# Performance work log

Hardware: AMD Instinct MI355X
Metric: run time of the kernel (lower is better)

The kernel has to match this reference:

```python
import jax, jax.numpy as jnp
import numpy as np

B, C, IMG, P = 8, 6, 384, 16
DIM, HEADS, DEPTH, MLP, NCLS = 768, 12, 4, 3072, 1000
N = (IMG // P) ** 2            # 576 patches
DH = DIM // HEADS              # 64
PATCH_DIM = C * P * P          # 1536


def setup_inputs() -> dict:
    key = jax.random.key(0)
    ks = jax.random.split(key, 13)
    f = lambda k, shp, s=0.02: jax.random.normal(k, shp, jnp.float32) * s
    return {
        "x": jax.random.normal(ks[0], (B, C, IMG, IMG), jnp.float32),
        "patch_w": f(ks[1], (PATCH_DIM, DIM)),
        "patch_b": f(ks[2], (DIM,)),
        "ln1_g": jnp.ones((DEPTH, DIM), jnp.float32),
        "ln1_b": jnp.zeros((DEPTH, DIM), jnp.float32),
        "w_qkv": f(ks[3], (DEPTH, DIM, 3 * DIM)),
        "bias_att": f(ks[4], (DEPTH, HEADS, N, N), 0.5),
        "w_out": f(ks[5], (DEPTH, DIM, DIM)),
        "ln2_g": jnp.ones((DEPTH, DIM), jnp.float32),
        "ln2_b": jnp.zeros((DEPTH, DIM), jnp.float32),
        "w1": f(ks[6], (DEPTH, DIM, MLP)),
        "b1": f(ks[7], (DEPTH, MLP)),
        "w2": f(ks[8], (DEPTH, MLP, DIM)),
        "b2": f(ks[9], (DEPTH, DIM)),
        "lnh_g": jnp.ones((DIM,), jnp.float32),
        "lnh_b": jnp.zeros((DIM,), jnp.float32),
        "w_head": f(ks[10], (DIM, NCLS)),
        "b_head": f(ks[11], (NCLS,)),
    }


def _ln(x, g, b, eps=1e-5):
    m = x.mean(-1, keepdims=True)
    v = ((x - m) ** 2).mean(-1, keepdims=True)
    return (x - m) * jax.lax.rsqrt(v + eps) * g + b


def _patchify(x, patch_w, patch_b):
    # Rearrange 'b c (h p1) (w p2) -> b (h w) (p1 p2 c)' then Linear(patch_dim, dim)
    b = x.shape[0]
    g = IMG // P
    x = x.reshape(b, C, g, P, g, P).transpose(0, 2, 4, 3, 5, 1).reshape(b, g * g, PATCH_DIM)
    return x @ patch_w + patch_b


def _forward(x, patch_w, patch_b, ln1_g, ln1_b, w_qkv, bias_att, w_out,
             ln2_g, ln2_b, w1, b1, w2, b2, lnh_g, lnh_b, w_head, b_head):
    scale = DH ** -0.5
    tok = _patchify(x, patch_w, patch_b)  # [B, N, DIM]; pos_info='mul_att_normed' -> no pos_embed added

    def block(t, p):
        l1g, l1b, wqkv, bias, wout, l2g, l2b, ww1, bb1, ww2, bb2 = p
        h = _ln(t, l1g, l1b)
        qkv = h @ wqkv                                     # [B, N, 3*DIM]
        q, k, v = jnp.split(qkv, 3, axis=-1)
        rs = lambda a: a.reshape(t.shape[0], N, HEADS, DH).transpose(0, 2, 1, 3)
        q, k, v = rs(q), rs(k), rs(v)                      # [B, H, N, DH]
        dots = jnp.einsum('bhid,bhjd->bhij', q, k) * scale
        # mul_att_normed: softmax(qk) * softmax(bias), renormalized over keys
        attn = jax.nn.softmax(dots, axis=-1) * jax.nn.softmax(bias, axis=-1)[None]
        attn = attn / attn.sum(-1, keepdims=True)
        o = jnp.einsum('bhij,bhjd->bhid', attn, v)
        o = o.transpose(0, 2, 1, 3).reshape(t.shape[0], N, DIM) @ wout
        t = t + o
        h2 = _ln(t, l2g, l2b)
        t = t + (jax.nn.gelu(h2 @ ww1 + bb1, approximate=False) @ ww2 + bb2)
        return t, None

    tok, _ = jax.lax.scan(block, tok,
                          (ln1_g, ln1_b, w_qkv, bias_att, w_out,
                           ln2_g, ln2_b, w1, b1, w2, b2))
    pooled = tok.mean(axis=1)                              # mean-pool tokens
    return _ln(pooled, lnh_g, lnh_b) @ w_head + b_head     # [B, NCLS]


def reference(x, patch_w, patch_b, ln1_g, ln1_b, w_qkv, bias_att, w_out,
              ln2_g, ln2_b, w1, b1, w2, b2, lnh_g, lnh_b, w_head, b_head):
    return _forward(x, patch_w, patch_b, ln1_g, ln1_b, w_qkv, bias_att, w_out,
                    ln2_g, ln2_b, w1, b1, w2, b2, lnh_g, lnh_b, w_head, b_head)
```

## Files before the change

### kernel.cpp

```cpp
#include <hip/hip_runtime.h>
#include <hip/hip_bf16.h>

typedef __attribute__((ext_vector_type(8))) short bf16x8;
typedef __attribute__((ext_vector_type(4))) float f32x4;

#define DEVI __device__ __forceinline__

DEVI unsigned short f2bf_bits(float f) {
    __hip_bfloat16 h = __float2bfloat16(f);
    return *reinterpret_cast<unsigned short*>(&h);
}
DEVI float bfbits2f(unsigned short u) {
    __hip_bfloat16 h = *reinterpret_cast<__hip_bfloat16*>(&u);
    return __bfloat162float(h);
}

DEVI void gload_lds16(const void* g, void* lds) {
    __builtin_amdgcn_global_load_lds(
        (const __attribute__((address_space(1))) unsigned int*)g,
        (__attribute__((address_space(3))) unsigned int*)lds, 16, 0, 0);
}

template <int N> DEVI void wait_vm() {
    if constexpr (N == 0) asm volatile("s_waitcnt vmcnt(0)" ::: "memory");
    else if constexpr (N == 6) asm volatile("s_waitcnt vmcnt(6)" ::: "memory");
    else if constexpr (N == 12) asm volatile("s_waitcnt vmcnt(12)" ::: "memory");
    __builtin_amdgcn_sched_barrier(0);
}

DEVI int2 remap2d(int bid, int total, int gx) {
    int q = total >> 3, r = total & 7, x = bid & 7, l = bid >> 3;
    int seq = (x < r ? x * (q + 1) : r * (q + 1) + (x - r) * q) + l;
    int g4 = seq / (4 * gx);
    int rem = seq - g4 * 4 * gx;
    return {g4 * 4 + (rem & 3), rem >> 2};
}

__global__ __launch_bounds__(256) void patchify_kernel(const float* __restrict__ x,
                                                       unsigned short* __restrict__ patches)
{
    size_t t8 = (size_t)blockIdx.x * 256 + threadIdx.x;
    int jq = (int)(t8 % 48);
    size_t t = t8 / 48;
    int r = (int)(t % 384); t /= 384;
    int c = (int)(t % 6);
    int b = (int)(t / 6);
    int j = jq * 8;
    int gh = r >> 4, p1 = r & 15, gw = j >> 4, p2 = j & 15;
    int prow = b * 576 + gh * 24 + gw;
    int pcol = c * 256 + p1 * 16 + p2;
    const float* src = x + ((((size_t)b * 6 + c) * 384 + r) * 384 + j);
    float4 v0 = ((const float4*)src)[0];
    float4 v1 = ((const float4*)src)[1];
    ushort u[8] = { f2bf_bits(v0.x), f2bf_bits(v0.y), f2bf_bits(v0.z), f2bf_bits(v0.w),
                    f2bf_bits(v1.x), f2bf_bits(v1.y), f2bf_bits(v1.z), f2bf_bits(v1.w) };
    *(int4*)&patches[(size_t)prow * 1536 + pcol] = *(int4*)u;
}

__global__ __launch_bounds__(256) void convT_patch_kernel(const float* __restrict__ W,
                                                          __hip_bfloat16* __restrict__ Wt)
{
    __shared__ float tile[32][33];
    int n0 = blockIdx.x * 32, kp0 = blockIdx.y * 32;
    int tx = threadIdx.x & 31, ty = threadIdx.x >> 5;
#pragma unroll
    for (int i = 0; i < 4; i++) {
        int kp = kp0 + ty + 8 * i;
        int k = (kp & 255) * 6 + (kp >> 8);
        tile[ty + 8 * i][tx] = W[(size_t)k * 768 + n0 + tx];
    }
    __syncthreads();
#pragma unroll
    for (int i = 0; i < 4; i++)
        Wt[(size_t)(n0 + ty + 8 * i) * 1536 + kp0 + tx] = __float2bfloat16(tile[tx][ty + 8 * i]);
}

DEVI void convT_body(const float* __restrict__ W, __hip_bfloat16* __restrict__ Wt,
                     int K, int N, int k0, int n0, int tid)
{
    __shared__ float tile[32][33];
    int tx = tid & 31, ty = tid >> 5;
#pragma unroll
    for (int i = 0; i < 4; i++)
        tile[ty + 8 * i][tx] = W[(size_t)(k0 + ty + 8 * i) * N + n0 + tx];
    __syncthreads();
#pragma unroll
    for (int i = 0; i < 4; i++)
        Wt[(size_t)(n0 + ty + 8 * i) * K + k0 + tx] = __float2bfloat16(tile[tx][ty + 8 * i]);
}

__global__ __launch_bounds__(256) void convT4_kernel(const float* __restrict__ wqkv,
                                                     const float* __restrict__ wout,
                                                     const float* __restrict__ w1,
                                                     const float* __restrict__ w2,
                                                     __hip_bfloat16* __restrict__ dst)
{
    int bt = blockIdx.x;
    const float* W; __hip_bfloat16* Wt; int K, N, lt;
    if (bt < 1728)      { W = wqkv; K = 768;  N = 2304; lt = bt;        Wt = dst; }
    else if (bt < 2304) { W = wout; K = 768;  N = 768;  lt = bt - 1728; Wt = dst + 1769472; }
    else if (bt < 4608) { W = w1;   K = 768;  N = 3072; lt = bt - 2304; Wt = dst + 2359296; }
    else                { W = w2;   K = 3072; N = 768;  lt = bt - 4608; Wt = dst + 4718592; }
    int tn = N >> 5;
    convT_body(W, Wt, K, N, (lt / tn) * 32, (lt % tn) * 32, threadIdx.x);
}

DEVI float ld_ln(const float* p) { return *p; }
DEVI float ld_ln(const __hip_bfloat16* p) { return __bfloat162float(*p); }
DEVI void st_ln(float* p, float v) { *p = v; }
DEVI void st_ln(__hip_bfloat16* p, float v) { *p = __float2bfloat16(v); }

template <typename InT, typename OutT>
__global__ __launch_bounds__(256) void ln_kernel(const InT* __restrict__ x,
                                                 const float* __restrict__ g,
                                                 const float* __restrict__ b,
                                                 OutT* __restrict__ out)
{
    int row = blockIdx.x, tid = threadIdx.x;
    const InT* xr = x + (size_t)row * 768;
    float v0 = ld_ln(&xr[tid]), v1 = ld_ln(&xr[tid + 256]), v2 = ld_ln(&xr[tid + 512]);
    float s = v0 + v1 + v2;
    float s2 = v0 * v0 + v1 * v1 + v2 * v2;
#pragma unroll
    for (int m = 32; m >= 1; m >>= 1) { s += __shfl_xor(s, m); s2 += __shfl_xor(s2, m); }
    __shared__ float red[8];
    int w = tid >> 6;
    if ((tid & 63) == 0) { red[w] = s; red[4 + w] = s2; }
    __syncthreads();
    s = red[0] + red[1] + red[2] + red[3];
    s2 = red[4] + red[5] + red[6] + red[7];
    float mean = s * (1.0f / 768.0f);
    float var = s2 * (1.0f / 768.0f) - mean * mean;
    float rstd = rsqrtf(var + 1e-5f);
    OutT* orow = out + (size_t)row * 768;
    st_ln(&orow[tid], (v0 - mean) * rstd * g[tid] + b[tid]);
    st_ln(&orow[tid + 256], (v1 - mean) * rstd * g[tid + 256] + b[tid + 256]);
    st_ln(&orow[tid + 512], (v2 - mean) * rstd * g[tid + 512] + b[tid + 512]);
}

template <bool BIAS, bool RESID>
__global__ __launch_bounds__(256, 2) void gemm_bt_kernel(
    const __hip_bfloat16* __restrict__ A,
    const __hip_bfloat16* __restrict__ Bt,
    const float* __restrict__ bias,
    const __hip_bfloat16* __restrict__ resid,
    __hip_bfloat16* __restrict__ Cb,
    int M, int N, int K, int gx)
{
    constexpr int BM = 64, SL = 6;
    __shared__ __align__(16) __hip_bfloat16 As[3][BM * 64];
    __shared__ __align__(16) __hip_bfloat16 Bs[3][128 * 64];
    const int tid = threadIdx.x;
    const int wid = tid >> 6, lane = tid & 63;
    const int g = lane >> 4, l16 = lane & 15;
    const int wm = (wid >> 1) * 32, wn = (wid & 1) * 64;

    int2 bc = remap2d(blockIdx.x, gridDim.x, gx);
    const int bm = bc.x * BM, bn = bc.y * 128;

    const int sr32 = tid >> 3, ci = tid & 7;
    const int cg = ci ^ (sr32 & 7);
    const int sdst = tid * 8;
    size_t aOff[2], bOff[4];
#pragma unroll
    for (int i = 0; i < 2; i++) aOff[i] = (size_t)(bm + i * 32 + sr32) * K + cg * 8;
#pragma unroll
    for (int i = 0; i < 4; i++) bOff[i] = (size_t)(bn + i * 32 + sr32) * K + cg * 8;

    auto stage = [&](__hip_bfloat16* asb, __hip_bfloat16* bsb, int tq) {
        const __hip_bfloat16* ap = A + tq * 64;
        const __hip_bfloat16* bp = Bt + tq * 64;
#pragma unroll
        for (int i = 0; i < 2; i++) gload_lds16(ap + aOff[i], asb + i * 2048 + sdst);
#pragma unroll
        for (int i = 0; i < 4; i++) gload_lds16(bp + bOff[i], bsb + i * 2048 + sdst);
    };

    f32x4 acc[2][4] = {};
    const int nt = K >> 6;

    stage(As[0], Bs[0], 0);
    stage(As[1], Bs[1], 1);
    stage(As[2], Bs[2], 2);
    wait_vm<2 * SL>();
    __builtin_amdgcn_s_barrier();
    __builtin_amdgcn_sched_barrier(0);

    for (int t = 0; t < nt; t += 3) {
#pragma unroll
        for (int u = 0; u < 3; u++) {
            const int tc = t + u;
            bf16x8 af[2][2], bfr[2][4];
#pragma unroll
            for (int s = 0; s < 2; s++) {
                const int cp = ((s * 4 + g) ^ (l16 & 7)) << 3;
#pragma unroll
                for (int mi = 0; mi < 2; mi++)
                    af[s][mi] = *(const bf16x8*)&As[u][(wm + mi * 16 + l16) * 64 + cp];
#pragma unroll
                for (int ni = 0; ni < 4; ni++)
                    bfr[s][ni] = *(const bf16x8*)&Bs[u][(wn + ni * 16 + l16) * 64 + cp];
            }
#pragma unroll
            for (int s = 0; s < 2; s++)
#pragma unroll
                for (int mi = 0; mi < 2; mi++)
#pragma unroll
                    for (int ni = 0; ni < 4; ni++)
                        acc[mi][ni] = __builtin_amdgcn_mfma_f32_16x16x32_bf16(af[s][mi], bfr[s][ni], acc[mi][ni], 0, 0, 0);

            asm volatile("s_waitcnt lgkmcnt(0)" ::: "memory");
            __builtin_amdgcn_sched_barrier(0);
            __builtin_amdgcn_s_barrier();
            __builtin_amdgcn_sched_barrier(0);

            if (tc + 3 < nt) stage(As[u], Bs[u], tc + 3);
            if (tc + 1 < nt) {
                if (tc + 4 <= nt)      wait_vm<2 * SL>();
                else if (tc + 3 == nt) wait_vm<SL>();
                else                   wait_vm<0>();
                __builtin_amdgcn_s_barrier();
                __builtin_amdgcn_sched_barrier(0);
            }
        }
    }

    __hip_bfloat16* scr = &As[0][0] + wid * (16 * 72);
#pragma unroll
    for (int mi = 0; mi < 2; mi++) {
#pragma unroll
        for (int ni = 0; ni < 4; ni++) {
            float bval = 0.0f;
            if (BIAS) bval = bias[bn + wn + ni * 16 + l16];
#pragma unroll
            for (int r = 0; r < 4; r++)
                scr[(4 * g + r) * 72 + ni * 16 + l16] = __float2bfloat16(acc[mi][ni][r] + bval);
        }
        asm volatile("s_waitcnt lgkmcnt(0)" ::: "memory");
        __builtin_amdgcn_sched_barrier(0);
#pragma unroll
        for (int q2 = 0; q2 < 2; q2++) {
            int row16 = q2 * 8 + (lane >> 3), ch = lane & 7;
            bf16x8 vv = *(const bf16x8*)&scr[row16 * 72 + ch * 8];
            int grow = bm + wm + mi * 16 + row16;
            size_t off = (size_t)grow * N + bn + wn + ch * 8;
            if (RESID) {
                bf16x8 rv = *(const bf16x8*)&resid[off];
#pragma unroll
                for (int e = 0; e < 8; e++)
                    vv[e] = (short)f2bf_bits(bfbits2f((unsigned short)vv[e]) + bfbits2f((unsigned short)rv[e]));
            }
            *(int4*)&Cb[off] = *(int4*)&vv;
        }
        asm volatile("s_waitcnt lgkmcnt(0)" ::: "memory");
        __builtin_amdgcn_sched_barrier(0);
    }
}

template <bool BIAS, bool GELU>
__global__ __launch_bounds__(256, 2) void gemm_wide_kernel(
    const __hip_bfloat16* __restrict__ A,
    const __hip_bfloat16* __restrict__ Bt,
    const float* __restrict__ bias,
    __hip_bfloat16* __restrict__ Cb,
    int M, int N, int K, int gx)
{
    constexpr int SL = 6;
    __shared__ __align__(16) __hip_bfloat16 As[3][128 * 32];
    __shared__ __align__(16) __hip_bfloat16 Bs[3][256 * 32];
    const int tid = threadIdx.x;
    const int wid = tid >> 6, lane = tid & 63;
    const int g = lane >> 4, l16 = lane & 15;
    const int wm = (wid >> 1) * 64, wn = (wid & 1) * 128;

    int2 bc = remap2d(blockIdx.x, gridDim.x, gx);
    const int bm = bc.x * 128, bn = bc.y * 256;

    const int sr = tid >> 2;
    const int csrc = (lane & 3) ^ ((lane >> 3) & 3);
    const int sdst = sr * 32 + (lane & 3) * 8;
    size_t aOff[2], bOff[4];
#pragma unroll
    for (int i = 0; i < 2; i++) aOff[i] = (size_t)(bm + i * 64 + sr) * K + csrc * 8;
#pragma unroll
    for (int i = 0; i < 4; i++) bOff[i] = (size_t)(bn + i * 64 + sr) * K + csrc * 8;

    auto stage = [&](__hip_bfloat16* asb, __hip_bfloat16* bsb, int tq) {
        const __hip_bfloat16* ap = A + tq * 32;
        const __hip_bfloat16* bp = Bt + tq * 32;
#pragma unroll
        for (int i = 0; i < 2; i++) gload_lds16(ap + aOff[i], asb + i * 2048 + sdst);
#pragma unroll
        for (int i = 0; i < 4; i++) gload_lds16(bp + bOff[i], bsb + i * 2048 + sdst);
    };

    const int pSw = (l16 >> 1) & 3;
    f32x4 acc[4][8] = {};
    const int nt = K >> 5;

    stage(As[0], Bs[0], 0);
    stage(As[1], Bs[1], 1);
    stage(As[2], Bs[2], 2);
    wait_vm<2 * SL>();
    __builtin_amdgcn_s_barrier();
    __builtin_amdgcn_sched_barrier(0);

    for (int t = 0; t < nt; t += 3) {
#pragma unroll
        for (int u = 0; u < 3; u++) {
            const int tc = t + u;
            bf16x8 af[4], bfr[8];
#pragma unroll
            for (int mi = 0; mi < 4; mi++)
                af[mi] = *(const bf16x8*)&As[u][(wm + mi * 16 + l16) * 32 + ((g ^ pSw) << 3)];
#pragma unroll
            for (int ni = 0; ni < 8; ni++)
                bfr[ni] = *(const bf16x8*)&Bs[u][(wn + ni * 16 + l16) * 32 + ((g ^ pSw) << 3)];
#pragma unroll
            for (int mi = 0; mi < 4; mi++)
#pragma unroll
                for (int ni = 0; ni < 8; ni++)
                    acc[mi][ni] = __builtin_amdgcn_mfma_f32_16x16x32_bf16(af[mi], bfr[ni], acc[mi][ni], 0, 0, 0);

            asm volatile("s_waitcnt lgkmcnt(0)" ::: "memory");
            __builtin_amdgcn_sched_barrier(0);
            __builtin_amdgcn_s_barrier();
            __builtin_amdgcn_sched_barrier(0);

            if (tc + 3 < nt) stage(As[u], Bs[u], tc + 3);
            if (tc + 1 < nt) {
                if (tc + 4 <= nt)      wait_vm<2 * SL>();
                else if (tc + 3 == nt) wait_vm<SL>();
                else                   wait_vm<0>();
                __builtin_amdgcn_s_barrier();
                __builtin_amdgcn_sched_barrier(0);
            }
        }
    }

    __hip_bfloat16* scr = &As[0][0] + wid * (16 * 136);
#pragma unroll
    for (int mi = 0; mi < 4; mi++) {
#pragma unroll
        for (int ni = 0; ni < 8; ni++) {
            float bval = 0.0f;
            if (BIAS) bval = bias[bn + wn + ni * 16 + l16];
#pragma unroll
            for (int r = 0; r < 4; r++) {
                float v = acc[mi][ni][r] + bval;
                if (GELU) v = 0.5f * v * (1.0f + erff(v * 0.70710678118654752f));
                scr[(4 * g + r) * 136 + ni * 16 + l16] = __float2bfloat16(v);
            }
        }
        asm volatile("s_waitcnt lgkmcnt(0)" ::: "memory");
        __builtin_amdgcn_sched_barrier(0);
#pragma unroll
        for (int q2 = 0; q2 < 4; q2++) {
            int idx = q2 * 64 + lane;
            int row16 = idx >> 4, ch = idx & 15;
            bf16x8 vv = *(const bf16x8*)&scr[row16 * 136 + ch * 8];
            int grow = bm + wm + mi * 16 + row16;
            *(int4*)&Cb[(size_t)grow * N + bn + wn + ch * 8] = *(int4*)&vv;
        }
        asm volatile("s_waitcnt lgkmcnt(0)" ::: "memory");
        __builtin_amdgcn_sched_barrier(0);
    }
}

__global__ __launch_bounds__(256) void attn_kernel(const __hip_bfloat16* __restrict__ qkvb,
                                                   const float* __restrict__ bias,
                                                   unsigned short* __restrict__ o)
{
    const int seq = (blockIdx.x & 7) * 108 + (blockIdx.x >> 3);
    const int bb = seq & 7, qt = (seq >> 3) % 9, h = seq / 72;
    const int q0 = qt * 64;
    const int tid = threadIdx.x;
    const int wq = tid >> 6, lane = tid & 63, g = lane >> 4, l16 = lane & 15;

    __shared__ __align__(16) unsigned short Qs[64 * 72];
    __shared__ __align__(16) unsigned short Ks[64 * 72];
    __shared__ __align__(16) unsigned short Vt[64 * 72];
    __shared__ __align__(16) unsigned short Ps[4][16 * 72];

    {
        int r = tid >> 2, cb = (tid & 3) * 16;
        const int4* s4 = (const int4*)&qkvb[(size_t)(bb * 576 + q0 + r) * 2304 + h * 64 + cb];
        int4* d4 = (int4*)&Qs[r * 72 + cb];
        d4[0] = s4[0]; d4[1] = s4[1];
    }
    __syncthreads();
    bf16x8 qf0 = *(const bf16x8*)&Qs[(wq * 16 + l16) * 72 + g * 8];
    bf16x8 qf1 = *(const bf16x8*)&Qs[(wq * 16 + l16) * 72 + 32 + g * 8];

    float m_r[4] = {-1e30f, -1e30f, -1e30f, -1e30f};
    float l_r[4] = {0.f, 0.f, 0.f, 0.f};
    f32x4 oa[4] = {};
    const float* bias_h = bias + (size_t)h * 576 * 576;
    const float scale = 0.125f;

    for (int kt = 0; kt < 576; kt += 64) {
        {
            int r = tid >> 2, cb = (tid & 3) * 16;
            const int4* s4 = (const int4*)&qkvb[(size_t)(bb * 576 + kt + r) * 2304 + 768 + h * 64 + cb];
            int4* d4 = (int4*)&Ks[r * 72 + cb];
            d4[0] = s4[0]; d4[1] = s4[1];
            int key = tid & 63, d0 = (tid >> 6) * 16;
            const unsigned short* vs = (const unsigned short*)&qkvb[(size_t)(bb * 576 + kt + key) * 2304 + 1536 + h * 64 + d0];
            bf16x8 v0 = *(const bf16x8*)vs;
            bf16x8 v1 = *(const bf16x8*)(vs + 8);
#pragma unroll
            for (int e = 0; e < 8; e++) {
                Vt[(d0 + e) * 72 + key] = (unsigned short)v0[e];
                Vt[(d0 + 8 + e) * 72 + key] = (unsigned short)v1[e];
            }
        }
        __syncthreads();

        float bl[4][4];
#pragma unroll
        for (int kc = 0; kc < 4; kc++)
#pragma unroll
            for (int r = 0; r < 4; r++) {
                int q = q0 + wq * 16 + 4 * g + r;
                bl[kc][r] = bias_h[(size_t)q * 576 + kt + kc * 16 + l16];
            }

        f32x4 sc[4] = {};
        __builtin_amdgcn_s_setprio(1);
#pragma unroll
        for (int kc = 0; kc < 4; kc++) {
            bf16x8 kf0 = *(const bf16x8*)&Ks[(kc * 16 + l16) * 72 + g * 8];
            bf16x8 kf1 = *(const bf16x8*)&Ks[(kc * 16 + l16) * 72 + 32 + g * 8];
            sc[kc] = __builtin_amdgcn_mfma_f32_16x16x32_bf16(qf0, kf0, sc[kc], 0, 0, 0);
            sc[kc] = __builtin_amdgcn_mfma_f32_16x16x32_bf16(qf1, kf1, sc[kc], 0, 0, 0);
        }
        __builtin_amdgcn_s_setprio(0);

        float sv[4][4], mt[4] = {-1e30f, -1e30f, -1e30f, -1e30f};
#pragma unroll
        for (int kc = 0; kc < 4; kc++)
#pragma unroll
            for (int r = 0; r < 4; r++) {
                float s = sc[kc][r] * scale + bl[kc][r];
                sv[kc][r] = s;
                mt[r] = fmaxf(mt[r], s);
            }
#pragma unroll
        for (int r = 0; r < 4; r++)
#pragma unroll
            for (int m = 1; m < 16; m <<= 1) mt[r] = fmaxf(mt[r], __shfl_xor(mt[r], m));

        float sf[4];
#pragma unroll
        for (int r = 0; r < 4; r++) {
            float mn = fmaxf(m_r[r], mt[r]);
            sf[r] = __expf(m_r[r] - mn);
            m_r[r] = mn;
        }
        float rs[4] = {0.f, 0.f, 0.f, 0.f};
#pragma unroll
        for (int kc = 0; kc < 4; kc++)
#pragma unroll
            for (int r = 0; r < 4; r++) {
                float p = __expf(sv[kc][r] - m_r[r]);
                rs[r] += p;
                Ps[wq][(4 * g + r) * 72 + kc * 16 + l16] = f2bf_bits(p);
            }
#pragma unroll
        for (int r = 0; r < 4; r++) {
#pragma unroll
            for (int m = 1; m < 16; m <<= 1) rs[r] += __shfl_xor(rs[r], m);
            l_r[r] = l_r[r] * sf[r] + rs[r];
        }
#pragma unroll
        for (int dt = 0; dt < 4; dt++)
#pragma unroll
            for (int r = 0; r < 4; r++) oa[dt][r] *= sf[r];

        asm volatile("s_waitcnt lgkmcnt(0)" ::: "memory");

        __builtin_amdgcn_s_setprio(1);
#pragma unroll
        for (int s = 0; s < 2; s++) {
            bf16x8 pf = *(const bf16x8*)&Ps[wq][l16 * 72 + s * 32 + g * 8];
#pragma unroll
            for (int dt = 0; dt < 4; dt++) {
                bf16x8 vf = *(const bf16x8*)&Vt[(dt * 16 + l16) * 72 + s * 32 + g * 8];
                oa[dt] = __builtin_amdgcn_mfma_f32_16x16x32_bf16(pf, vf, oa[dt], 0, 0, 0);
            }
        }
        __builtin_amdgcn_s_setprio(0);
        __syncthreads();
    }

#pragma unroll
    for (int dt = 0; dt < 4; dt++)
#pragma unroll
        for (int r = 0; r < 4; r++) {
            int q = q0 + wq * 16 + 4 * g + r;
            float v = oa[dt][r] / l_r[r];
            o[(size_t)(bb * 576 + q) * 768 + h * 64 + dt * 16 + l16] = f2bf_bits(v);
        }
}

__global__ __launch_bounds__(256) void pool_kernel(const __hip_bfloat16* __restrict__ tok,
                                                   float* __restrict__ pooled)
{
    int d = blockIdx.x * 256 + threadIdx.x;
    int b = blockIdx.y;
    float s = 0.0f;
    for (int n = 0; n < 576; n++) s += __bfloat162float(tok[(size_t)(b * 576 + n) * 768 + d]);
    pooled[b * 768 + d] = s * (1.0f / 576.0f);
}

__global__ __launch_bounds__(256) void head_kernel(const float* __restrict__ lnp,
                                                   const float* __restrict__ w,
                                                   const float* __restrict__ bh,
                                                   float* __restrict__ out)
{
    int c = blockIdx.x * 256 + threadIdx.x;
    int b = blockIdx.y;
    if (c >= 1000) return;
    float s = bh[c];
    for (int d = 0; d < 768; d++) s += lnp[b * 768 + d] * w[(size_t)d * 1000 + c];
    out[b * 1000 + c] = s;
}

extern "C" void kernel_launch(void* const* d_in, const int* in_sizes, int n_in,
                              void* d_out, int out_size, void* d_ws, size_t ws_size,
                              hipStream_t stream)
{
    const float* x = (const float*)d_in[0];
    const float* patch_w = (const float*)d_in[1];
    const float* patch_b = (const float*)d_in[2];
    const float* ln1_g = (const float*)d_in[3];
    const float* ln1_b = (const float*)d_in[4];
    const float* w_qkv = (const float*)d_in[5];
    const float* bias_att = (const float*)d_in[6];
    const float* w_out = (const float*)d_in[7];
    const float* ln2_g = (const float*)d_in[8];
    const float* ln2_b = (const float*)d_in[9];
    const float* w1 = (const float*)d_in[10];
    const float* b1 = (const float*)d_in[11];
    const float* w2 = (const float*)d_in[12];
    const float* b2 = (const float*)d_in[13];
    const float* lnh_g = (const float*)d_in[14];
    const float* lnh_b = (const float*)d_in[15];
    const float* w_head = (const float*)d_in[16];
    const float* b_head = (const float*)d_in[17];
    float* out = (float*)d_out;

    char* ws = (char*)d_ws;
    __hip_bfloat16* tok = (__hip_bfloat16*)(ws + 0);
    __hip_bfloat16* qkv_bf = (__hip_bfloat16*)(ws + 14155776);
    float* pooled = (float*)(ws + 56623104);
    float* pooledln = (float*)(ws + 56647680);
    __hip_bfloat16* patches = (__hip_bfloat16*)(ws + 56672256);
    __hip_bfloat16* lw = patches;
    __hip_bfloat16* h_bf = (__hip_bfloat16*)(ws + 70828032);
    __hip_bfloat16* o_bf = (__hip_bfloat16*)(ws + 77905920);
    __hip_bfloat16* hid_bf = (__hip_bfloat16*)(ws + 84983808);
    __hip_bfloat16* wbuf = (__hip_bfloat16*)(ws + 113295360);

    patchify_kernel<<<3456, 256, 0, stream>>>(x, (unsigned short*)patches);
    convT_patch_kernel<<<dim3(24, 48), 256, 0, stream>>>(patch_w, wbuf);
    gemm_bt_kernel<true, false><<<432, 256, 0, stream>>>(
        patches, wbuf, patch_b, nullptr, tok, 4608, 768, 1536, 6);

    for (int l = 0; l < 4; l++) {
        convT4_kernel<<<6912, 256, 0, stream>>>(
            w_qkv + (size_t)l * 768 * 2304, w_out + (size_t)l * 768 * 768,
            w1 + (size_t)l * 768 * 3072, w2 + (size_t)l * 3072 * 768, lw);
        ln_kernel<__hip_bfloat16, __hip_bfloat16><<<4608, 256, 0, stream>>>(
            tok, ln1_g + l * 768, ln1_b + l * 768, h_bf);
        gemm_wide_kernel<false, false><<<324, 256, 0, stream>>>(
            h_bf, lw, nullptr, qkv_bf, 4608, 2304, 768, 9);
        attn_kernel<<<864, 256, 0, stream>>>(
            qkv_bf, bias_att + (size_t)l * 12 * 576 * 576, (unsigned short*)o_bf);
        gemm_bt_kernel<false, true><<<432, 256, 0, stream>>>(
            o_bf, lw + 1769472, nullptr, tok, tok, 4608, 768, 768, 6);
        ln_kernel<__hip_bfloat16, __hip_bfloat16><<<4608, 256, 0, stream>>>(
            tok, ln2_g + l * 768, ln2_b + l * 768, h_bf);
        gemm_wide_kernel<true, true><<<432, 256, 0, stream>>>(
            h_bf, lw + 2359296, b1 + l * 3072, hid_bf, 4608, 3072, 768, 12);
        gemm_bt_kernel<true, true><<<432, 256, 0, stream>>>(
            hid_bf, lw + 4718592, b2 + l * 768, tok, tok, 4608, 768, 3072, 6);
    }

    pool_kernel<<<dim3(3, 8), 256, 0, stream>>>(tok, pooled);
    ln_kernel<float, float><<<8, 256, 0, stream>>>(pooled, lnh_g, lnh_b, pooledln);
    head_kernel<<<dim3(4, 8), 256, 0, stream>>>(pooledln, w_head, b_head, out);
}
```

Baseline: 845.4 us.

## Replace wide GEMM with 256x256 eight-wave ping-pong pipelined GEMM kernel

Adds gemm_8ph_kernel, a 512-thread, 256x256-tile GEMM that splits each K=64 step into two 32-wide halves in double-buffered LDS. It interleaves global-to-LDS staging of the next halves with four MFMA phases, separated by barriers and s_setprio. It replaces gemm_wide_kernel for the QKV and MLP-up GEMMs, halving the block count. The goal is more reuse per tile and overlap of loads with compute. The cost is fewer blocks (162/216 on 256 CUs, under one wave) and a heavier register footprint.

```diff
diff --git a/kernel.cpp b/kernel.cpp
--- a/kernel.cpp
+++ b/kernel.cpp
@@ -23,8 +23,13 @@
 
 template <int N> DEVI void wait_vm() {
     if constexpr (N == 0) asm volatile("s_waitcnt vmcnt(0)" ::: "memory");
+    else if constexpr (N == 4) asm volatile("s_waitcnt vmcnt(4)" ::: "memory");
     else if constexpr (N == 6) asm volatile("s_waitcnt vmcnt(6)" ::: "memory");
     else if constexpr (N == 12) asm volatile("s_waitcnt vmcnt(12)" ::: "memory");
+    __builtin_amdgcn_sched_barrier(0);
+}
+DEVI void lgkm0() {
+    asm volatile("s_waitcnt lgkmcnt(0)" ::: "memory");
     __builtin_amdgcn_sched_barrier(0);
 }
 
@@ -34,6 +39,13 @@
     int g4 = seq / (4 * gx);
     int rem = seq - g4 * 4 * gx;
     return {g4 * 4 + (rem & 3), rem >> 2};
+}
+DEVI int2 remap2d_g2(int bid, int total, int gx) {
+    int q = total >> 3, r = total & 7, x = bid & 7, l = bid >> 3;
+    int seq = (x < r ? x * (q + 1) : r * (q + 1) + (x - r) * q) + l;
+    int g2 = seq / (2 * gx);
+    int rem = seq - g2 * 2 * gx;
+    return {g2 * 2 + (rem & 1), rem >> 1};
 }
 
 __global__ __launch_bounds__(256) void patchify_kernel(const float* __restrict__ x,
@@ -138,6 +150,152 @@
     st_ln(&orow[tid + 512], (v2 - mean) * rstd * g[tid + 512] + b[tid + 512]);
 }
 
+template <bool BIAS, bool GELU>
+__global__ __launch_bounds__(512, 2) void gemm_8ph_kernel(
+    const __hip_bfloat16* __restrict__ A,
+    const __hip_bfloat16* __restrict__ Bt,
+    const float* __restrict__ bias,
+    __hip_bfloat16* __restrict__ Cb,
+    int M, int N, int K, int gx)
+{
+    __shared__ __align__(16) __hip_bfloat16 AsF[32768];
+    __shared__ __align__(16) __hip_bfloat16 BsF[32768];
+    const int tid = threadIdx.x;
+    const int wid = tid >> 6, lane = tid & 63;
+    const int g = lane >> 4, l16 = lane & 15;
+    const int wmh = wid >> 2, wnn = wid & 3;
+
+    int2 bc = remap2d_g2(blockIdx.x, gridDim.x, gx);
+    const int bm = bc.x * 256, bn = bc.y * 256;
+
+    const int srow = tid >> 2;
+    size_t aS[2], bS[2];
+#pragma unroll
+    for (int i = 0; i < 2; i++) {
+        int row = i * 128 + srow;
+        int lc = (tid & 3) ^ ((row >> 1) & 3);
+        aS[i] = (size_t)(bm + row) * K + lc * 8;
+        bS[i] = (size_t)(bn + row) * K + lc * 8;
+    }
+    auto stageA = [&](int buf, int kh, int tq) {
+        const __hip_bfloat16* ap = A + (size_t)tq * 64 + kh * 32;
+        __hip_bfloat16* dst = AsF + (buf * 2 + kh) * 8192;
+        gload_lds16(ap + aS[0], dst + tid * 8);
+        gload_lds16(ap + aS[1], dst + 4096 + tid * 8);
+    };
+    auto stageB = [&](int buf, int kh, int tq) {
+        const __hip_bfloat16* bp = Bt + (size_t)tq * 64 + kh * 32;
+        __hip_bfloat16* dst = BsF + (buf * 2 + kh) * 8192;
+        gload_lds16(bp + bS[0], dst + tid * 8);
+        gload_lds16(bp + bS[1], dst + 4096 + tid * 8);
+    };
+
+    const int csw = (l16 >> 1) & 3;
+    const int rdo = (g ^ csw) << 3;
+    const int aBase = (wmh * 128 + l16) * 32 + rdo;
+    const int bBase = (wnn * 64 + l16) * 32 + rdo;
+
+    f32x4 acc[8][4] = {};
+    const int nt = K >> 6;
+
+    stageA(0, 0, 0); stageB(0, 0, 0); stageA(0, 1, 0); stageB(0, 1, 0);
+    stageA(1, 0, 1); stageB(1, 0, 1);
+    wait_vm<4>();
+    __builtin_amdgcn_s_barrier();
+    __builtin_amdgcn_sched_barrier(0);
+
+    bf16x8 af[8], bf2[2];
+    for (int t = 0; t < nt; t++) {
+        const int b = t & 1;
+        const int k0 = (b * 2 + 0) * 8192, k1 = (b * 2 + 1) * 8192;
+
+#pragma unroll
+        for (int mi = 0; mi < 8; mi++) af[mi] = *(const bf16x8*)&AsF[k0 + aBase + mi * 512];
+        bf2[0] = *(const bf16x8*)&BsF[k0 + bBase + 0 * 512];
+        bf2[1] = *(const bf16x8*)&BsF[k0 + bBase + 1 * 512];
+        if (t + 1 < nt) stageA(b ^ 1, 1, t + 1);
+        __builtin_amdgcn_s_barrier(); lgkm0();
+        __builtin_amdgcn_s_setprio(1);
+#pragma unroll
+        for (int mi = 0; mi < 8; mi++) {
+            acc[mi][0] = __builtin_amdgcn_mfma_f32_16x16x32_bf16(af[mi], bf2[0], acc[mi][0], 0, 0, 0);
+            acc[mi][1] = __builtin_amdgcn_mfma_f32_16x16x32_bf16(af[mi], bf2[1], acc[mi][1], 0, 0, 0);
+        }
+        __builtin_amdgcn_s_setprio(0);
+        __builtin_amdgcn_s_barrier();
+
+        bf2[0] = *(const bf16x8*)&BsF[k0 + bBase + 2 * 512];
+        bf2[1] = *(const bf16x8*)&BsF[k0 + bBase + 3 * 512];
+        if (t + 1 < nt) stageB(b ^ 1, 1, t + 1);
+        __builtin_amdgcn_s_barrier(); lgkm0();
+        __builtin_amdgcn_s_setprio(1);
+#pragma unroll
+        for (int mi = 0; mi < 8; mi++) {
+            acc[mi][2] = __builtin_amdgcn_mfma_f32_16x16x32_bf16(af[mi], bf2[0], acc[mi][2], 0, 0, 0);
+            acc[mi][3] = __builtin_amdgcn_mfma_f32_16x16x32_bf16(af[mi], bf2[1], acc[mi][3], 0, 0, 0);
+        }
+        __builtin_amdgcn_s_setprio(0);
+        __builtin_amdgcn_s_barrier();
+
+#pragma unroll
+        for (int mi = 0; mi < 8; mi++) af[mi] = *(const bf16x8*)&AsF[k1 + aBase + mi * 512];
+        bf2[0] = *(const bf16x8*)&BsF[k1 + bBase + 0 * 512];
+        bf2[1] = *(const bf16x8*)&BsF[k1 + bBase + 1 * 512];
+        if (t + 2 < nt) stageA(b, 0, t + 2);
+        __builtin_amdgcn_s_barrier(); lgkm0();
+        __builtin_amdgcn_s_setprio(1);
+#pragma unroll
+        for (int mi = 0; mi < 8; mi++) {
+            acc[mi][0] = __builtin_amdgcn_mfma_f32_16x16x32_bf16(af[mi], bf2[0], acc[mi][0], 0, 0, 0);
+            acc[mi][1] = __builtin_amdgcn_mfma_f32_16x16x32_bf16(af[mi], bf2[1], acc[mi][1], 0, 0, 0);
+        }
+        __builtin_amdgcn_s_setprio(0);
+        __builtin_amdgcn_s_barrier();
+
+        bf2[0] = *(const bf16x8*)&BsF[k1 + bBase + 2 * 512];
+        bf2[1] = *(const bf16x8*)&BsF[k1 + bBase + 3 * 512];
+        if (t + 2 < nt) stageB(b, 0, t + 2);
+        __builtin_amdgcn_s_barrier(); lgkm0();
+        __builtin_amdgcn_s_setprio(1);
+#pragma unroll
+        for (int mi = 0; mi < 8; mi++) {
+            acc[mi][2] = __builtin_amdgcn_mfma_f32_16x16x32_bf16(af[mi], bf2[0], acc[mi][2], 0, 0, 0);
+            acc[mi][3] = __builtin_amdgcn_mfma_f32_16x16x32_bf16(af[mi], bf2[1], acc[mi][3], 0, 0, 0);
+        }
+        __builtin_amdgcn_s_setprio(0);
+        if (t + 2 < nt) wait_vm<4>();
+        else            wait_vm<0>();
+        __builtin_amdgcn_s_barrier();
+        __builtin_amdgcn_sched_barrier(0);
+    }
+
+    __hip_bfloat16* scr = AsF + wid * (16 * 72);
+#pragma unroll
+    for (int mi = 0; mi < 8; mi++) {
+#pragma unroll
+        for (int ni = 0; ni < 4; ni++) {
+            float bval = 0.0f;
+            if (BIAS) bval = bias[bn + wnn * 64 + ni * 16 + l16];
+#pragma unroll
+            for (int r = 0; r < 4; r++) {
+                float v = acc[mi][ni][r] + bval;
+                if (GELU) v = 0.5f * v * (1.0f + erff(v * 0.70710678118654752f));
+                scr[(4 * g + r) * 72 + ni * 16 + l16] = __float2bfloat16(v);
+            }
+        }
+        lgkm0();
+#pragma unroll
+        for (int q2 = 0; q2 < 2; q2++) {
+            int idx = q2 * 64 + lane;
+            int row16 = idx >> 3, ch = idx & 7;
+            bf16x8 vv = *(const bf16x8*)&scr[row16 * 72 + ch * 8];
+            int grow = bm + wmh * 128 + mi * 16 + row16;
+            *(int4*)&Cb[(size_t)grow * N + bn + wnn * 64 + ch * 8] = *(int4*)&vv;
+        }
+        lgkm0();
+    }
+}
+
 template <bool BIAS, bool RESID>
 __global__ __launch_bounds__(256, 2) void gemm_bt_kernel(
     const __hip_bfloat16* __restrict__ A,
@@ -182,7 +340,7 @@
     stage(As[0], Bs[0], 0);
     stage(As[1], Bs[1], 1);
     stage(As[2], Bs[2], 2);
-    wait_vm<2 * SL>();
+    wait_vm<12>();
     __builtin_amdgcn_s_barrier();
     __builtin_amdgcn_sched_barrier(0);
 
@@ -209,15 +367,14 @@
                     for (int ni = 0; ni < 4; ni++)
                         acc[mi][ni] = __builtin_amdgcn_mfma_f32_16x16x32_bf16(af[s][mi], bfr[s][ni], acc[mi][ni], 0, 0, 0);
 
-            asm volatile("s_waitcnt lgkmcnt(0)" ::: "memory");
-            __builtin_amdgcn_sched_barrier(0);
+            lgkm0();
             __builtin_amdgcn_s_barrier();
             __builtin_amdgcn_sched_barrier(0);
 
             if (tc + 3 < nt) stage(As[u], Bs[u], tc + 3);
             if (tc + 1 < nt) {
-                if (tc + 4 <= nt)      wait_vm<2 * SL>();
-                else if (tc + 3 == nt) wait_vm<SL>();
+                if (tc + 4 <= nt)      wait_vm<12>();
+                else if (tc + 3 == nt) wait_vm<6>();
                 else                   wait_vm<0>();
                 __builtin_amdgcn_s_barrier();
                 __builtin_amdgcn_sched_barrier(0);
@@ -236,8 +393,7 @@
             for (int r = 0; r < 4; r++)
                 scr[(4 * g + r) * 72 + ni * 16 + l16] = __float2bfloat16(acc[mi][ni][r] + bval);
         }
-        asm volatile("s_waitcnt lgkmcnt(0)" ::: "memory");
-        __builtin_amdgcn_sched_barrier(0);
+        lgkm0();
 #pragma unroll
         for (int q2 = 0; q2 < 2; q2++) {
             int row16 = q2 * 8 + (lane >> 3), ch = lane & 7;
@@ -252,118 +408,7 @@
             }
             *(int4*)&Cb[off] = *(int4*)&vv;
         }
-        asm volatile("s_waitcnt lgkmcnt(0)" ::: "memory");
-        __builtin_amdgcn_sched_barrier(0);
-    }
-}
-
-template <bool BIAS, bool GELU>
-__global__ __launch_bounds__(256, 2) void gemm_wide_kernel(
-    const __hip_bfloat16* __restrict__ A,
-    const __hip_bfloat16* __restrict__ Bt,
-    const float* __restrict__ bias,
-    __hip_bfloat16* __restrict__ Cb,
-    int M, int N, int K, int gx)
-{
-    constexpr int SL = 6;
-    __shared__ __align__(16) __hip_bfloat16 As[3][128 * 32];
-    __shared__ __align__(16) __hip_bfloat16 Bs[3][256 * 32];
-    const int tid = threadIdx.x;
-    const int wid = tid >> 6, lane = tid & 63;
-    const int g = lane >> 4, l16 = lane & 15;
-    const int wm = (wid >> 1) * 64, wn = (wid & 1) * 128;
-
-    int2 bc = remap2d(blockIdx.x, gridDim.x, gx);
-    const int bm = bc.x * 128, bn = bc.y * 256;
-
-    const int sr = tid >> 2;
-    const int csrc = (lane & 3) ^ ((lane >> 3) & 3);
-    const int sdst = sr * 32 + (lane & 3) * 8;
-    size_t aOff[2], bOff[4];
-#pragma unroll
-    for (int i = 0; i < 2; i++) aOff[i] = (size_t)(bm + i * 64 + sr) * K + csrc * 8;
-#pragma unroll
-    for (int i = 0; i < 4; i++) bOff[i] = (size_t)(bn + i * 64 + sr) * K + csrc * 8;
-
-    auto stage = [&](__hip_bfloat16* asb, __hip_bfloat16* bsb, int tq) {
-        const __hip_bfloat16* ap = A + tq * 32;
-        const __hip_bfloat16* bp = Bt + tq * 32;
-#pragma unroll
-        for (int i = 0; i < 2; i++) gload_lds16(ap + aOff[i], asb + i * 2048 + sdst);
-#pragma unroll
-        for (int i = 0; i < 4; i++) gload_lds16(bp + bOff[i], bsb + i * 2048 + sdst);
-    };
-
-    const int pSw = (l16 >> 1) & 3;
-    f32x4 acc[4][8] = {};
-    const int nt = K >> 5;
-
-    stage(As[0], Bs[0], 0);
-    stage(As[1], Bs[1], 1);
-    stage(As[2], Bs[2], 2);
-    wait_vm<2 * SL>();
-    __builtin_amdgcn_s_barrier();
-    __builtin_amdgcn_sched_barrier(0);
-
-    for (int t = 0; t < nt; t += 3) {
-#pragma unroll
-        for (int u = 0; u < 3; u++) {
-            const int tc = t + u;
-            bf16x8 af[4], bfr[8];
-#pragma unroll
-            for (int mi = 0; mi < 4; mi++)
-                af[mi] = *(const bf16x8*)&As[u][(wm + mi * 16 + l16) * 32 + ((g ^ pSw) << 3)];
-#pragma unroll
-            for (int ni = 0; ni < 8; ni++)
-                bfr[ni] = *(const bf16x8*)&Bs[u][(wn + ni * 16 + l16) * 32 + ((g ^ pSw) << 3)];
-#pragma unroll
-            for (int mi = 0; mi < 4; mi++)
-#pragma unroll
-                for (int ni = 0; ni < 8; ni++)
-                    acc[mi][ni] = __builtin_amdgcn_mfma_f32_16x16x32_bf16(af[mi], bfr[ni], acc[mi][ni], 0, 0, 0);
-
-            asm volatile("s_waitcnt lgkmcnt(0)" ::: "memory");
-            __builtin_amdgcn_sched_barrier(0);
-            __builtin_amdgcn_s_barrier();
-            __builtin_amdgcn_sched_barrier(0);
-
-            if (tc + 3 < nt) stage(As[u], Bs[u], tc + 3);
-            if (tc + 1 < nt) {
-                if (tc + 4 <= nt)      wait_vm<2 * SL>();
-                else if (tc + 3 == nt) wait_vm<SL>();
-                else                   wait_vm<0>();
-                __builtin_amdgcn_s_barrier();
-                __builtin_amdgcn_sched_barrier(0);
-            }
-        }
-    }
-
-    __hip_bfloat16* scr = &As[0][0] + wid * (16 * 136);
-#pragma unroll
-    for (int mi = 0; mi < 4; mi++) {
-#pragma unroll
-        for (int ni = 0; ni < 8; ni++) {
-            float bval = 0.0f;
-            if (BIAS) bval = bias[bn + wn + ni * 16 + l16];
-#pragma unroll
-            for (int r = 0; r < 4; r++) {
-                float v = acc[mi][ni][r] + bval;
-                if (GELU) v = 0.5f * v * (1.0f + erff(v * 0.70710678118654752f));
-                scr[(4 * g + r) * 136 + ni * 16 + l16] = __float2bfloat16(v);
-            }
-        }
-        asm volatile("s_waitcnt lgkmcnt(0)" ::: "memory");
-        __builtin_amdgcn_sched_barrier(0);
-#pragma unroll
-        for (int q2 = 0; q2 < 4; q2++) {
-            int idx = q2 * 64 + lane;
-            int row16 = idx >> 4, ch = idx & 15;
-            bf16x8 vv = *(const bf16x8*)&scr[row16 * 136 + ch * 8];
-            int grow = bm + wm + mi * 16 + row16;
-            *(int4*)&Cb[(size_t)grow * N + bn + wn + ch * 8] = *(int4*)&vv;
-        }
-        asm volatile("s_waitcnt lgkmcnt(0)" ::: "memory");
-        __builtin_amdgcn_sched_barrier(0);
+        lgkm0();
     }
 }
 
@@ -573,7 +618,7 @@
             w1 + (size_t)l * 768 * 3072, w2 + (size_t)l * 3072 * 768, lw);
         ln_kernel<__hip_bfloat16, __hip_bfloat16><<<4608, 256, 0, stream>>>(
             tok, ln1_g + l * 768, ln1_b + l * 768, h_bf);
-        gemm_wide_kernel<false, false><<<324, 256, 0, stream>>>(
+        gemm_8ph_kernel<false, false><<<162, 512, 0, stream>>>(
             h_bf, lw, nullptr, qkv_bf, 4608, 2304, 768, 9);
         attn_kernel<<<864, 256, 0, stream>>>(
             qkv_bf, bias_att + (size_t)l * 12 * 576 * 576, (unsigned short*)o_bf);
@@ -581,7 +626,7 @@
             o_bf, lw + 1769472, nullptr, tok, tok, 4608, 768, 768, 6);
         ln_kernel<__hip_bfloat16, __hip_bfloat16><<<4608, 256, 0, stream>>>(
             tok, ln2_g + l * 768, ln2_b + l * 768, h_bf);
-        gemm_wide_kernel<true, true><<<432, 256, 0, stream>>>(
+        gemm_8ph_kernel<true, true><<<216, 512, 0, stream>>>(
             h_bf, lw + 2359296, b1 + l * 3072, hid_bf, 4608, 3072, 768, 12);
         gemm_bt_kernel<true, true><<<432, 256, 0, stream>>>(
             hid_bf, lw + 4718592, b2 + l * 768, tok, tok, 4608, 768, 3072, 6);
```

New measurement: 835.7 us. About the same (-1.1%).
